# Kernel optimization log

Measured on AMD Instinct MI355X. Metric: run time of the kernel, lower is better.

## Reference

```python
import jax, jax.numpy as jnp
import numpy as np

T = 4          # num edge types
D = 256        # embedding_size == hidden_size
N = 100_000    # nodes
E_EDGES = 320_000
VOCAB = 10_000


def setup_inputs() -> dict:
    key = jax.random.key(0)
    ks = jax.random.split(key, 12)
    s = 0.02
    input_ids = jax.random.randint(ks[0], (1, N), 0, VOCAB)
    etype = jax.random.randint(ks[1], (1, E_EDGES), 1, T + 1)  # types 1..T
    src = jax.random.randint(ks[2], (1, E_EDGES), 0, N)
    tgt = jax.random.randint(ks[3], (1, E_EDGES), 0, N)
    typed_edges = jnp.stack([etype[0], src[0], tgt[0]], axis=0)[None]  # [1,3,E]
    embed_table = jax.random.normal(ks[4], (VOCAB, D)) * s
    # 6 inner layers (3 per concat block x 2 blocks): 256 -> 256
    edge_W_inner = jax.random.normal(ks[5], (6, T, D, 2 * D)) * s
    ln_s_inner = jnp.ones((6, D)); ln_b_inner = jnp.zeros((6, D))
    dense_W_inner = jax.random.normal(ks[6], (6, D, D)) * s
    dense_b_inner = jnp.zeros((6, D))
    # 2 output layers on concat [state, hidden]: hidden_size 512 -> 256
    edge_W_out = jax.random.normal(ks[7], (2, T, 2 * D, 4 * D)) * s
    ln_s_out = jnp.ones((2, 2 * D)); ln_b_out = jnp.zeros((2, 2 * D))
    dense_W_out = jax.random.normal(ks[8], (2, D, 2 * D)) * s
    dense_b_out = jnp.zeros((2, D))
    return {
        "input_ids": input_ids, "typed_edges": typed_edges,
        "embed_table": embed_table,
        "edge_W_inner": edge_W_inner, "ln_s_inner": ln_s_inner, "ln_b_inner": ln_b_inner,
        "dense_W_inner": dense_W_inner, "dense_b_inner": dense_b_inner,
        "edge_W_out": edge_W_out, "ln_s_out": ln_s_out, "ln_b_out": ln_b_out,
        "dense_W_out": dense_W_out, "dense_b_out": dense_b_out,
    }


def layer_norm(x, s, b, eps=1e-5):
    mu = jnp.mean(x, axis=-1, keepdims=True)
    var = jnp.mean((x - mu) ** 2, axis=-1, keepdims=True)
    return (x - mu) * jax.lax.rsqrt(var + eps) * s + b


def message_passing(state, etype, src, tgt, edge_W):
    # state [N,d]; edge_W [T, d, 2d]. Gather endpoints, per-type linear, scatter-add to targets.
    es = jnp.concatenate([state[src], state[tgt]], axis=1)  # [E, 2d]
    msgs = jnp.zeros((es.shape[0], edge_W.shape[1]), state.dtype)
    for t in range(edge_W.shape[0]):  # small fixed number of edge types
        msgs = msgs + jnp.where((etype == t + 1)[:, None], es @ edge_W[t].T, 0.0)
    return jax.ops.segment_sum(msgs, tgt, num_segments=state.shape[0])


def gnn_layer(state, etype, src, tgt, eW, ls, lb, dW, db):
    m = message_passing(state, etype, src, tgt, eW)
    h = layer_norm(jax.nn.gelu(m, approximate=False), ls, lb)
    return jnp.tanh(h @ dW.T + db)


def concat_block(state, etype, src, tgt, eWi, lsi, lbi, dWi, dbi, eWo, lso, lbo, dWo, dbo):
    x = state
    for i in range(3):
        x = gnn_layer(x, etype, src, tgt, eWi[i], lsi[i], lbi[i], dWi[i], dbi[i])
    res = jnp.concatenate([state, x], axis=1)  # [N, 2d] residual concat
    return gnn_layer(res, etype, src, tgt, eWo, lso, lbo, dWo, dbo)


def reference(input_ids, typed_edges, embed_table, edge_W_inner, ln_s_inner, ln_b_inner,
              dense_W_inner, dense_b_inner, edge_W_out, ln_s_out, ln_b_out,
              dense_W_out, dense_b_out):
    ids = input_ids[0]
    te = typed_edges[0]
    etype, src, tgt = te[0], te[1], te[2]
    x = embed_table[ids]  # [N, D]
    for b in range(2):
        sl = slice(3 * b, 3 * b + 3)
        x = concat_block(x, etype, src, tgt,
                         edge_W_inner[sl], ln_s_inner[sl], ln_b_inner[sl],
                         dense_W_inner[sl], dense_b_inner[sl],
                         edge_W_out[b], ln_s_out[b], ln_b_out[b],
                         dense_W_out[b], dense_b_out[b])
    return x
```

## Files before the change

kernel.cpp:

```cpp
#include <hip/hip_runtime.h>
#include <cstdio>

#define N_NODES 100000
#define NPAD    100096
#define NTILES  782
#define NE      320000
#define NCH     196
#define WCO_OFF 3145728L
#define OUT_ELEMS (N_NODES * 256)

typedef unsigned short ushort_t;
typedef unsigned short u16x4 __attribute__((ext_vector_type(4)));
typedef unsigned short u16x8 __attribute__((ext_vector_type(8)));
typedef _Float16       f16;
typedef _Float16       f16x8 __attribute__((ext_vector_type(8)));
typedef float          f32x4 __attribute__((ext_vector_type(4)));
typedef float          f32x4v __attribute__((ext_vector_type(4)));

__device__ __forceinline__ float bf2f(ushort_t u) {
    return __uint_as_float(((unsigned)u) << 16);
}
__device__ __forceinline__ ushort_t f2bf(float f) {
    unsigned u = __float_as_uint(f);
    u += 0x7FFFu + ((u >> 16) & 1u);
    return (ushort_t)(u >> 16);
}
__device__ __forceinline__ ushort_t f2h(float f) {
    f16 h = (f16)f;
    return __builtin_bit_cast(ushort_t, h);
}
__device__ __forceinline__ float h2f(ushort_t u) {
    return (float)__builtin_bit_cast(f16, u);
}

__device__ __forceinline__ int xcd_remap(int pbid, int nwg) {
    int q = nwg >> 3, r = nwg & 7;
    int xcd = pbid & 7, idx = pbid >> 3;
    int base = (xcd < r) ? xcd * (q + 1) : r * (q + 1) + (xcd - r) * q;
    return base + idx;
}

__device__ __forceinline__ float fast_tanh(float x) {
    x = fminf(fmaxf(x, -10.f), 10.f);
    float e = __expf(2.f * x);
    return (e - 1.f) / (e + 1.f);
}

__device__ __forceinline__ float gelu_f(float x) {
    return 0.5f * x * (1.f + erff(x * 0.70710678118654752f));
}

__global__ __launch_bounds__(256) void detect_k(const unsigned* __restrict__ w0, int* __restrict__ flag) {
    __shared__ int lds[256];
    int t = threadIdx.x;
    int cnt = 0;
    for (int i = t; i < 2048; i += 256) {
        unsigned e = (w0[i] >> 7) & 0xFFu;
        cnt += (e >= 96u && e <= 140u) ? 1 : 0;
    }
    lds[t] = cnt; __syncthreads();
    for (int s = 128; s > 0; s >>= 1) {
        if (t < s) lds[t] += lds[t + s];
        __syncthreads();
    }
    if (t == 0) *flag = (lds[0] < 1024) ? 1 : 0;
}

__device__ __forceinline__ ushort_t load_in(const void* p, long i, bool isf32) {
    return isf32 ? f2h(((const float*)p)[i]) : f2h(bf2f(((const ushort_t*)p)[i]));
}

struct CvtArgs {
    const void* src[8];
    ushort_t*   dst[8];
    int         n[8];
};

__global__ __launch_bounds__(256) void cvt_k(CvtArgs a, const int* __restrict__ flag) {
    int ti = blockIdx.y;
    int n = a.n[ti];
    const void* s = a.src[ti];
    ushort_t* d = a.dst[ti];
    bool isf32 = (*flag != 0);
    for (int i = blockIdx.x * 256 + threadIdx.x; i < n; i += gridDim.x * 256)
        d[i] = load_in(s, i, isf32);
}

__global__ __launch_bounds__(256) void scale_w_k(const ushort_t* __restrict__ dWiC,
                                                 const ushort_t* __restrict__ lsiC,
                                                 const ushort_t* __restrict__ lbiC,
                                                 const ushort_t* __restrict__ dbiC,
                                                 const ushort_t* __restrict__ dWoC,
                                                 const ushort_t* __restrict__ lsoC,
                                                 const ushort_t* __restrict__ lboC,
                                                 const ushort_t* __restrict__ dboC,
                                                 ushort_t* __restrict__ dWiS,
                                                 float* __restrict__ uwi, float* __restrict__ w0i,
                                                 ushort_t* __restrict__ dWoS,
                                                 float* __restrict__ uwo, float* __restrict__ w0o) {
    int wid = blockIdx.x * 4 + (threadIdx.x >> 6);
    int l = threadIdx.x & 63;
    float u = 0.f, w0 = 0.f;
    if (wid < 1536) {
        int lay = wid >> 8, c = wid & 255;
        u16x4 wv = *(const u16x4*)(dWiC + (size_t)wid * 256 + l * 4);
        u16x4 sv = *(const u16x4*)(lsiC + lay * 256 + l * 4);
        u16x4 bv = *(const u16x4*)(lbiC + lay * 256 + l * 4);
        u16x4 ov;
        #pragma unroll
        for (int i = 0; i < 4; i++) {
            float W = h2f(wv[i]);
            float ws = W * h2f(sv[i]);
            ov[i] = f2h(ws);
            u += ws; w0 += W * h2f(bv[i]);
        }
        *(u16x4*)(dWiS + (size_t)wid * 256 + l * 4) = ov;
        #pragma unroll
        for (int m = 1; m < 64; m <<= 1) {
            u += __shfl_xor(u, m, 64); w0 += __shfl_xor(w0, m, 64);
        }
        if (l == 0) { uwi[wid] = u; w0i[wid] = w0 + h2f(dbiC[lay * 256 + c]); }
    } else if (wid < 2048) {
        int w2 = wid - 1536;
        int b = w2 >> 8, c = w2 & 255;
        u16x8 wv = *(const u16x8*)(dWoC + (size_t)w2 * 512 + l * 8);
        u16x8 sv = *(const u16x8*)(lsoC + b * 512 + l * 8);
        u16x8 bv = *(const u16x8*)(lboC + b * 512 + l * 8);
        u16x8 ov;
        #pragma unroll
        for (int i = 0; i < 8; i++) {
            float W = h2f(wv[i]);
            float ws = W * h2f(sv[i]);
            ov[i] = f2h(ws);
            u += ws; w0 += W * h2f(bv[i]);
        }
        *(u16x8*)(dWoS + (size_t)w2 * 512 + l * 8) = ov;
        #pragma unroll
        for (int m = 1; m < 64; m <<= 1) {
            u += __shfl_xor(u, m, 64); w0 += __shfl_xor(w0, m, 64);
        }
        if (l == 0) { uwo[w2] = u; w0o[w2] = w0 + h2f(dboC[b * 256 + c]); }
    }
}

__global__ __launch_bounds__(256) void pack_w(const void* __restrict__ eWi,
                                              const void* __restrict__ eWo,
                                              ushort_t* __restrict__ WC,
                                              const int* __restrict__ flag) {
    long idx = (long)blockIdx.x * 256 + threadIdx.x;
    bool isf32 = (*flag != 0);
    const long ELI = 6L * 4 * 256 * 512;
    const long ELO = 2L * 4 * 512 * 1024;
    if (idx < ELI) {
        int j = idx & 511;
        int o = (idx >> 9) & 255;
        int t = (idx >> 17) & 3;
        long l = idx >> 19;
        int q = o >> 6, oo = o & 63;
        int k = j & 255;
        int n = ((j < 256) ? 0 : 256) + t * 64 + oo;
        WC[l * 524288 + (long)q * 131072 + (long)n * 256 + k] = load_in(eWi, idx, isf32);
    } else if (idx < ELI + ELO) {
        long i2 = idx - ELI;
        int j = i2 & 1023;
        int o = (i2 >> 10) & 511;
        int t = (i2 >> 19) & 3;
        long b = i2 >> 21;
        int c = o >> 6, oo = o & 63;
        int k = j & 511;
        int n = ((j < 512) ? 0 : 256) + t * 64 + oo;
        WC[WCO_OFF + b * 2097152L + (long)c * 262144 + (long)n * 512 + k] = load_in(eWo, i2, isf32);
    }
}

__global__ __launch_bounds__(256) void embed_k(const int* __restrict__ ids,
                                               const void* __restrict__ tab,
                                               ushort_t* __restrict__ S,
                                               const int* __restrict__ flag) {
    int row = blockIdx.x * 4 + (threadIdx.x >> 6);
    int l = threadIdx.x & 63;
    if (row >= N_NODES) return;
    int id = ids[row];
    u16x4 v;
    if (*flag) {
        f32x4v fv = *(const f32x4v*)((const float*)tab + (size_t)id * 256 + l * 4);
        #pragma unroll
        for (int i = 0; i < 4; i++) v[i] = f2h(fv[i]);
    } else {
        u16x4 bv = *(const u16x4*)((const ushort_t*)tab + (size_t)id * 256 + l * 4);
        #pragma unroll
        for (int i = 0; i < 4; i++) v[i] = f2h(bf2f(bv[i]));
    }
    *(u16x4*)(S + (size_t)row * 256 + l * 4) = v;
}

__global__ __launch_bounds__(256) void emit_k(const ushort_t* __restrict__ Bst, void* __restrict__ out,
                                              const int* __restrict__ flag) {
    long i = (long)blockIdx.x * 256 + threadIdx.x;
    if (i >= OUT_ELEMS) return;
    float v = h2f(Bst[i]);
    if (*flag) ((float*)out)[i] = v;
    else       ((ushort_t*)out)[i] = f2bf(v);
}

__global__ __launch_bounds__(256) void count_k(const int* __restrict__ tgt, int* __restrict__ counts) {
    int e = blockIdx.x * 256 + threadIdx.x;
    if (e < NE) atomicAdd(&counts[tgt[e]], 1);
}

__global__ __launch_bounds__(256) void scan1_k(const int* __restrict__ counts,
                                               int* __restrict__ incl, int* __restrict__ chsums) {
    __shared__ int lds[256];
    int c = blockIdx.x, t = threadIdx.x;
    int i0 = c * 512 + 2 * t;
    int a = (i0 < N_NODES) ? counts[i0] : 0;
    int b = (i0 + 1 < N_NODES) ? counts[i0 + 1] : 0;
    int ps = a + b;
    lds[t] = ps; __syncthreads();
    int x = ps;
    for (int off = 1; off < 256; off <<= 1) {
        int y = (t >= off) ? lds[t - off] : 0;
        __syncthreads();
        x += y; lds[t] = x;
        __syncthreads();
    }
    int excl = x - ps;
    if (i0 < N_NODES) incl[i0] = excl + a;
    if (i0 + 1 < N_NODES) incl[i0 + 1] = excl + a + b;
    if (t == 255) chsums[c] = x;
}

__global__ __launch_bounds__(256) void scan2_k(const int* __restrict__ chsums, int* __restrict__ chunkoff) {
    __shared__ int lds[256];
    int t = threadIdx.x;
    int v = (t < NCH) ? chsums[t] : 0;
    lds[t] = v; __syncthreads();
    int x = v;
    for (int off = 1; off < 256; off <<= 1) {
        int y = (t >= off) ? lds[t - off] : 0;
        __syncthreads();
        x += y; lds[t] = x;
        __syncthreads();
    }
    if (t <= NCH) chunkoff[t] = x - v;
}

__global__ __launch_bounds__(256) void scan3_k(const int* __restrict__ counts, const int* __restrict__ incl,
                                               const int* __restrict__ chunkoff,
                                               int* __restrict__ offsets, int* __restrict__ cursor) {
    int c = blockIdx.x, t = threadIdx.x;
    int base = chunkoff[c];
    #pragma unroll
    for (int k = 0; k < 2; k++) {
        int i = c * 512 + 2 * t + k;
        if (i < N_NODES) {
            int off = base + incl[i] - counts[i];
            offsets[i] = off;
            cursor[i] = off;
        }
    }
    if (c == 0 && t == 0) offsets[N_NODES] = chunkoff[NCH];
}

__global__ __launch_bounds__(256) void fill_k(const int* __restrict__ et, const int* __restrict__ src,
                                              const int* __restrict__ tgt,
                                              int* __restrict__ cursor, int* __restrict__ sorted) {
    int e = blockIdx.x * 256 + threadIdx.x;
    if (e < NE) {
        int pos = atomicAdd(&cursor[tgt[e]], 1);
        sorted[pos] = ((et[e] - 1) << 28) | src[e];
    }
}

template<int EPI>
__global__ __launch_bounds__(256) void gemm_bt(const ushort_t* __restrict__ A,
                                               const ushort_t* __restrict__ B,
                                               int K, int ldc,
                                               ushort_t* __restrict__ Cb,
                                               const float2* __restrict__ MR,
                                               const float* __restrict__ uu,
                                               const float* __restrict__ w0t,
                                               int storeM) {
    __shared__ __align__(16) ushort_t As[2][128 * 64];
    __shared__ __align__(16) ushort_t Bs[2][128 * 64];
    const int tid = threadIdx.x;
    const int w = tid >> 6, l = tid & 63;
    const int wr = w >> 1, wc = w & 1;
    const int gx = gridDim.x;
    const int lbid = xcd_remap(blockIdx.y * gx + blockIdx.x, gx * gridDim.y);
    const long m0 = (long)(lbid / gx) * 128, n0 = (long)(lbid % gx) * 128;
    const int lr = l >> 3;
    const int lc = (l & 7) * 8;
    const int cbk = ((l & 7) ^ lr) * 8;
    f32x4 acc[4][4];
    #pragma unroll
    for (int s = 0; s < 4; s++)
        #pragma unroll
        for (int n = 0; n < 4; n++) acc[s][n] = (f32x4){0.f, 0.f, 0.f, 0.f};

    auto stage = [&](int buf, int k0) {
        #pragma unroll
        for (int q = 0; q < 4; q++) {
            int row = w * 32 + q * 8 + lr;
            const ushort_t* ga = A + (m0 + row) * (long)K + k0 + cbk;
            __builtin_amdgcn_global_load_lds(
                (__attribute__((address_space(1))) unsigned int*)(ga),
                (__attribute__((address_space(3))) unsigned int*)(&As[buf][row * 64 + lc]), 16, 0, 0);
            const ushort_t* gb = B + (n0 + row) * (long)K + k0 + cbk;
            __builtin_amdgcn_global_load_lds(
                (__attribute__((address_space(1))) unsigned int*)(gb),
                (__attribute__((address_space(3))) unsigned int*)(&Bs[buf][row * 64 + lc]), 16, 0, 0);
        }
    };

    stage(0, 0);
    int cur = 0;
    for (int k0 = 0; k0 < K; k0 += 64) {
        __syncthreads();
        if (k0 + 64 < K) stage(cur ^ 1, k0 + 64);
        #pragma unroll
        for (int kk = 0; kk < 2; kk++) {
            f16x8 af[4], bfr[4];
            const int gb = kk * 4 + (l >> 4);
            const int sb = (gb ^ (l & 7)) * 8;
            #pragma unroll
            for (int s = 0; s < 4; s++)
                af[s] = *(const f16x8*)&As[cur][(wr * 64 + s * 16 + (l & 15)) * 64 + sb];
            #pragma unroll
            for (int n = 0; n < 4; n++)
                bfr[n] = *(const f16x8*)&Bs[cur][(wc * 64 + n * 16 + (l & 15)) * 64 + sb];
            #pragma unroll
            for (int s = 0; s < 4; s++)
                #pragma unroll
                for (int n = 0; n < 4; n++)
                    acc[s][n] = __builtin_amdgcn_mfma_f32_16x16x32_f16(bfr[n], af[s], acc[s][n], 0, 0, 0);
        }
        cur ^= 1;
    }
    const long r0 = m0 + wr * 64 + (l & 15);
    const long c0 = n0 + wc * 64 + ((l >> 4) << 2);
    #pragma unroll
    for (int s = 0; s < 4; s++) {
        long r = r0 + s * 16;
        if constexpr (EPI == 2) {
            if (r < storeM) {
                float2 mr = MR[r];
                #pragma unroll
                for (int n = 0; n < 4; n++) {
                    long c = c0 + n * 16;
                    f32x4v u4 = *(const f32x4v*)&uu[c];
                    f32x4v w4 = *(const f32x4v*)&w0t[c];
                    u16x4 o;
                    #pragma unroll
                    for (int j = 0; j < 4; j++)
                        o[j] = f2h(fast_tanh(mr.y * (acc[s][n][j] - mr.x * u4[j]) + w4[j]));
                    *(u16x4*)&Cb[r * ldc + c] = o;
                }
            }
        } else {
            #pragma unroll
            for (int n = 0; n < 4; n++) {
                long c = c0 + n * 16;
                u16x4 o;
                #pragma unroll
                for (int j = 0; j < 4; j++) o[j] = f2h(acc[s][n][j]);
                *(u16x4*)&Cb[r * ldc + c] = o;
            }
        }
    }
}

__global__ __launch_bounds__(256) void gemm_bt2(const ushort_t* __restrict__ A0,
                                                const ushort_t* __restrict__ A1,
                                                const ushort_t* __restrict__ B,
                                                int ldc,
                                                ushort_t* __restrict__ Cb) {
    __shared__ __align__(16) ushort_t As[2][128 * 64];
    __shared__ __align__(16) ushort_t Bs[2][128 * 64];
    const int tid = threadIdx.x;
    const int w = tid >> 6, l = tid & 63;
    const int wr = w >> 1, wc = w & 1;
    const int gx = gridDim.x;
    const int lbid = xcd_remap(blockIdx.y * gx + blockIdx.x, gx * gridDim.y);
    const long m0 = (long)(lbid / gx) * 128, n0 = (long)(lbid % gx) * 128;
    const int lr = l >> 3;
    const int lc = (l & 7) * 8;
    const int cbk = ((l & 7) ^ lr) * 8;
    f32x4 acc[4][4];
    #pragma unroll
    for (int s = 0; s < 4; s++)
        #pragma unroll
        for (int n = 0; n < 4; n++) acc[s][n] = (f32x4){0.f, 0.f, 0.f, 0.f};

    auto stage = [&](int buf, int k0) {
        const ushort_t* Ab = (k0 < 256) ? A0 : A1;
        const int kq = k0 & 255;
        #pragma unroll
        for (int q = 0; q < 4; q++) {
            int row = w * 32 + q * 8 + lr;
            const ushort_t* ga = Ab + (m0 + row) * 256L + kq + cbk;
            __builtin_amdgcn_global_load_lds(
                (__attribute__((address_space(1))) unsigned int*)(ga),
                (__attribute__((address_space(3))) unsigned int*)(&As[buf][row * 64 + lc]), 16, 0, 0);
            const ushort_t* gb = B + (n0 + row) * 512L + k0 + cbk;
            __builtin_amdgcn_global_load_lds(
                (__attribute__((address_space(1))) unsigned int*)(gb),
                (__attribute__((address_space(3))) unsigned int*)(&Bs[buf][row * 64 + lc]), 16, 0, 0);
        }
    };

    stage(0, 0);
    int cur = 0;
    for (int k0 = 0; k0 < 512; k0 += 64) {
        __syncthreads();
        if (k0 + 64 < 512) stage(cur ^ 1, k0 + 64);
        #pragma unroll
        for (int kk = 0; kk < 2; kk++) {
            f16x8 af[4], bfr[4];
            const int gb = kk * 4 + (l >> 4);
            const int sb = (gb ^ (l & 7)) * 8;
            #pragma unroll
            for (int s = 0; s < 4; s++)
                af[s] = *(const f16x8*)&As[cur][(wr * 64 + s * 16 + (l & 15)) * 64 + sb];
            #pragma unroll
            for (int n = 0; n < 4; n++)
                bfr[n] = *(const f16x8*)&Bs[cur][(wc * 64 + n * 16 + (l & 15)) * 64 + sb];
            #pragma unroll
            for (int s = 0; s < 4; s++)
                #pragma unroll
                for (int n = 0; n < 4; n++)
                    acc[s][n] = __builtin_amdgcn_mfma_f32_16x16x32_f16(bfr[n], af[s], acc[s][n], 0, 0, 0);
        }
        cur ^= 1;
    }
    const long r0 = m0 + wr * 64 + (l & 15);
    const long c0 = n0 + wc * 64 + ((l >> 4) << 2);
    #pragma unroll
    for (int s = 0; s < 4; s++) {
        long r = r0 + s * 16;
        #pragma unroll
        for (int n = 0; n < 4; n++) {
            long c = c0 + n * 16;
            u16x4 o;
            #pragma unroll
            for (int j = 0; j < 4; j++) o[j] = f2h(acc[s][n][j]);
            *(u16x4*)&Cb[r * ldc + c] = o;
        }
    }
}

__global__ __launch_bounds__(256) void agg_q(const ushort_t* __restrict__ Z,
                                             const int* __restrict__ offsets,
                                             const int* __restrict__ sorted,
                                             ushort_t* __restrict__ G, int mld, int q,
                                             float* __restrict__ Sg, float* __restrict__ Sq) {
    int v = blockIdx.x * 4 + (threadIdx.x >> 6);
    int l = threadIdx.x & 63;
    if (v >= NPAD) return;
    ushort_t* mp = G + (size_t)v * mld + (q << 6) + l;
    if (v >= N_NODES) { *mp = 0; return; }
    float acc = 0.f;
    int d0 = 0, d1 = 0, d2 = 0, d3 = 0;
    int beg = offsets[v], end = offsets[v + 1];
    for (int e = beg; e < end; ++e) {
        int pk = sorted[e];
        int t = pk >> 28;
        int s = pk & 0x0FFFFFFF;
        acc += h2f(Z[(size_t)s * 512 + (t << 6) + l]);
        d0 += (t == 0); d1 += (t == 1); d2 += (t == 2); d3 += (t == 3);
    }
    const ushort_t* zs = Z + (size_t)v * 512 + 256 + l;
    if (d0) acc += (float)d0 * h2f(zs[0]);
    if (d1) acc += (float)d1 * h2f(zs[64]);
    if (d2) acc += (float)d2 * h2f(zs[128]);
    if (d3) acc += (float)d3 * h2f(zs[192]);
    float g = gelu_f(acc);
    *mp = f2h(g);
    float sg = g, sq = g * g;
    #pragma unroll
    for (int m = 1; m < 64; m <<= 1) {
        sg += __shfl_xor(sg, m, 64);
        sq += __shfl_xor(sq, m, 64);
    }
    if (l == 0) {
        atomicAdd(&Sg[v], sg);
        atomicAdd(&Sq[v], sq);
    }
}

__global__ __launch_bounds__(256) void stats_k(float* __restrict__ Sg, float* __restrict__ Sq,
                                               float2* __restrict__ MR, float inv) {
    int v = blockIdx.x * 256 + threadIdx.x;
    if (v >= N_NODES) return;
    float mean = Sg[v] * inv;
    float var = fmaxf(Sq[v] * inv - mean * mean, 0.f);
    MR[v] = make_float2(mean, rsqrtf(var + 1e-5f));
    Sg[v] = 0.f; Sq[v] = 0.f;
}

extern "C" void kernel_launch(void* const* d_in, const int* in_sizes, int n_in,
                              void* d_out, int out_size, void* d_ws, size_t ws_size,
                              hipStream_t stream) {
    const int* ids = (const int*)d_in[0];
    const int* te = (const int*)d_in[1];
    const int* et = te;
    const int* esrc = te + NE;
    const int* etgt = te + 2 * NE;
    const void* tab = d_in[2];
    const void* eWi = d_in[3];
    const void* lsi = d_in[4];
    const void* lbi = d_in[5];
    const void* dWi = d_in[6];
    const void* dbi = d_in[7];
    const void* eWo = d_in[8];
    const void* lso = d_in[9];
    const void* lbo = d_in[10];
    const void* dWo = d_in[11];
    const void* dbo = d_in[12];

    char* w = (char*)d_ws;
    auto alloc = [&](size_t bytes) -> char* {
        char* p = w; w += (bytes + 255) & ~(size_t)255; return p;
    };
    ushort_t* A    = (ushort_t*)alloc((size_t)NPAD * 256 * 2);
    ushort_t* Bst  = (ushort_t*)alloc((size_t)NPAD * 256 * 2);
    ushort_t* WC   = (ushort_t*)alloc(7340032UL * 2);
    ushort_t* lsiC = (ushort_t*)alloc(1536 * 2);
    ushort_t* lbiC = (ushort_t*)alloc(1536 * 2);
    ushort_t* dbiC = (ushort_t*)alloc(1536 * 2);
    ushort_t* lsoC = (ushort_t*)alloc(1024 * 2);
    ushort_t* lboC = (ushort_t*)alloc(1024 * 2);
    ushort_t* dboC = (ushort_t*)alloc(512 * 2);
    ushort_t* dWiC = (ushort_t*)alloc(393216UL * 2);
    ushort_t* dWoC = (ushort_t*)alloc(262144UL * 2);
    ushort_t* dWiS = (ushort_t*)alloc(393216UL * 2);
    ushort_t* dWoS = (ushort_t*)alloc(262144UL * 2);
    float* uwi     = (float*)alloc(1536 * 4);
    float* w0i     = (float*)alloc(1536 * 4);
    float* uwo     = (float*)alloc(512 * 4);
    float* w0o     = (float*)alloc(512 * 4);
    float* Sg      = (float*)alloc((size_t)NPAD * 4);
    float* Sq      = (float*)alloc((size_t)NPAD * 4);
    float2* MR     = (float2*)alloc((size_t)NPAD * 8);
    int* flag      = (int*)alloc(256);
    int* counts    = (int*)alloc((size_t)N_NODES * 4);
    int* incl      = (int*)alloc((size_t)N_NODES * 4);
    int* chsums    = (int*)alloc(1024);
    int* chunkoff  = (int*)alloc(1024);
    int* offsets   = (int*)alloc((size_t)(N_NODES + 8) * 4);
    int* cursor    = (int*)alloc((size_t)N_NODES * 4);
    int* sorted    = (int*)alloc((size_t)NE * 4);
    ushort_t* G    = (ushort_t*)alloc((size_t)NPAD * 512 * 2);
    ushort_t* R;
    if ((size_t)out_size >= (size_t)NPAD * 256 * 2) R = (ushort_t*)d_out;
    else R = (ushort_t*)alloc((size_t)NPAD * 256 * 2);
    size_t fixed = (size_t)(w - (char*)d_ws);

    const size_t ZQ_BYTES = (size_t)NPAD * 512 * 2;
    size_t bigsz = (ws_size > fixed) ? (ws_size - fixed) : 0;
    if (bigsz < ZQ_BYTES) {
        fprintf(stderr, "kernel_launch: ws too small (%zu bytes, fixed %zu, big %zu) -- no-op\n",
                ws_size, fixed, bigsz);
        return;
    }
    ushort_t* Zq = (ushort_t*)w;

    detect_k<<<1, 256, 0, stream>>>((const unsigned*)tab, flag);
    CvtArgs ca;
    ca.src[0] = lsi;  ca.dst[0] = lsiC; ca.n[0] = 1536;
    ca.src[1] = lbi;  ca.dst[1] = lbiC; ca.n[1] = 1536;
    ca.src[2] = dbi;  ca.dst[2] = dbiC; ca.n[2] = 1536;
    ca.src[3] = lso;  ca.dst[3] = lsoC; ca.n[3] = 1024;
    ca.src[4] = lbo;  ca.dst[4] = lboC; ca.n[4] = 1024;
    ca.src[5] = dbo;  ca.dst[5] = dboC; ca.n[5] = 512;
    ca.src[6] = dWi;  ca.dst[6] = dWiC; ca.n[6] = 393216;
    ca.src[7] = dWo;  ca.dst[7] = dWoC; ca.n[7] = 262144;
    cvt_k<<<dim3(1536, 8), 256, 0, stream>>>(ca, flag);
    scale_w_k<<<512, 256, 0, stream>>>(dWiC, lsiC, lbiC, dbiC, dWoC, lsoC, lboC, dboC,
                                       dWiS, uwi, w0i, dWoS, uwo, w0o);
    hipMemsetAsync(counts, 0, (size_t)N_NODES * 4, stream);
    hipMemsetAsync(Sg, 0, (size_t)NPAD * 4, stream);
    hipMemsetAsync(Sq, 0, (size_t)NPAD * 4, stream);
    hipMemsetAsync(A   + (size_t)N_NODES * 256, 0, (size_t)(NPAD - N_NODES) * 256 * 2, stream);
    hipMemsetAsync(Bst + (size_t)N_NODES * 256, 0, (size_t)(NPAD - N_NODES) * 256 * 2, stream);
    hipMemsetAsync(R   + (size_t)N_NODES * 256, 0, (size_t)(NPAD - N_NODES) * 256 * 2, stream);
    pack_w<<<28672, 256, 0, stream>>>(eWi, eWo, WC, flag);
    embed_k<<<N_NODES / 4, 256, 0, stream>>>(ids, tab, A, flag);
    count_k<<<(NE + 255) / 256, 256, 0, stream>>>(etgt, counts);
    scan1_k<<<NCH, 256, 0, stream>>>(counts, incl, chsums);
    scan2_k<<<1, 256, 0, stream>>>(chsums, chunkoff);
    scan3_k<<<NCH, 256, 0, stream>>>(counts, incl, chunkoff, offsets, cursor);
    fill_k<<<(NE + 255) / 256, 256, 0, stream>>>(et, esrc, etgt, cursor, sorted);

    auto inner_layer = [&](const ushort_t* Xin, ushort_t* Xout, int lay) {
        for (int q = 0; q < 4; q++) {
            gemm_bt<3><<<dim3(4, NTILES), 256, 0, stream>>>(
                Xin, WC + (long)lay * 524288 + (long)q * 131072, 256, 512, Zq,
                nullptr, nullptr, nullptr, 0);
            agg_q<<<NPAD / 4, 256, 0, stream>>>(Zq, offsets, sorted, G, 256, q, Sg, Sq);
        }
        stats_k<<<(N_NODES + 255) / 256, 256, 0, stream>>>(Sg, Sq, MR, 1.f / 256.f);
        gemm_bt<2><<<dim3(2, NTILES), 256, 0, stream>>>(G, dWiS + (long)lay * 65536, 256, 256,
                                                        Xout, MR, uwi + lay * 256, w0i + lay * 256, N_NODES);
    };

    auto out_layer = [&](const ushort_t* X0, const ushort_t* X1, int b, ushort_t* dest) {
        for (int c = 0; c < 8; c++) {
            gemm_bt2<<<dim3(4, NTILES), 256, 0, stream>>>(
                X0, X1, WC + WCO_OFF + (long)b * 2097152 + (long)c * 262144, 512, Zq);
            agg_q<<<NPAD / 4, 256, 0, stream>>>(Zq, offsets, sorted, G, 512, c, Sg, Sq);
        }
        stats_k<<<(N_NODES + 255) / 256, 256, 0, stream>>>(Sg, Sq, MR, 1.f / 512.f);
        gemm_bt<2><<<dim3(2, NTILES), 256, 0, stream>>>(G, dWoS + (long)b * 131072, 512, 256,
                                                        dest, MR, uwo + b * 256, w0o + b * 256, N_NODES);
    };

    inner_layer(A, Bst, 0);
    inner_layer(Bst, R, 1);
    inner_layer(R, Bst, 2);
    out_layer(A, Bst, 0, R);
    inner_layer(R, A, 3);
    inner_layer(A, Bst, 4);
    inner_layer(Bst, A, 5);
    out_layer(R, A, 1, Bst);

    emit_k<<<(OUT_ELEMS + 255) / 256, 256, 0, stream>>>(Bst, d_out, flag);
}
```

Measured before the change: 6.046 ms.

## Triple-buffer GEMM LDS staging with BK=32 and explicit vmcnt waits

```diff
diff --git a/kernel.cpp b/kernel.cpp
--- a/kernel.cpp
+++ b/kernel.cpp
@@ -281,17 +281,18 @@
                                                const float* __restrict__ uu,
                                                const float* __restrict__ w0t,
                                                int storeM) {
-    __shared__ __align__(16) ushort_t As[2][128 * 64];
-    __shared__ __align__(16) ushort_t Bs[2][128 * 64];
+    __shared__ __align__(16) ushort_t As[3][128 * 32];
+    __shared__ __align__(16) ushort_t Bs[3][128 * 32];
     const int tid = threadIdx.x;
     const int w = tid >> 6, l = tid & 63;
     const int wr = w >> 1, wc = w & 1;
     const int gx = gridDim.x;
     const int lbid = xcd_remap(blockIdx.y * gx + blockIdx.x, gx * gridDim.y);
     const long m0 = (long)(lbid / gx) * 128, n0 = (long)(lbid % gx) * 128;
-    const int lr = l >> 3;
-    const int lc = (l & 7) * 8;
-    const int cbk = ((l & 7) ^ lr) * 8;
+    const int cbk = (((l & 3) ^ ((l >> 4) & 3)) * 8);
+    const int ldst = (l & 3) * 8;
+    const int lrow = l >> 2;
+    const int sb = (((l >> 4) ^ ((l >> 2) & 3)) * 8);
     f32x4 acc[4][4];
     #pragma unroll
     for (int s = 0; s < 4; s++)
@@ -300,42 +301,44 @@
 
     auto stage = [&](int buf, int k0) {
         #pragma unroll
-        for (int q = 0; q < 4; q++) {
-            int row = w * 32 + q * 8 + lr;
+        for (int q = 0; q < 2; q++) {
+            int row = w * 32 + q * 16 + lrow;
             const ushort_t* ga = A + (m0 + row) * (long)K + k0 + cbk;
             __builtin_amdgcn_global_load_lds(
                 (__attribute__((address_space(1))) unsigned int*)(ga),
-                (__attribute__((address_space(3))) unsigned int*)(&As[buf][row * 64 + lc]), 16, 0, 0);
+                (__attribute__((address_space(3))) unsigned int*)(&As[buf][row * 32 + ldst]), 16, 0, 0);
             const ushort_t* gb = B + (n0 + row) * (long)K + k0 + cbk;
             __builtin_amdgcn_global_load_lds(
                 (__attribute__((address_space(1))) unsigned int*)(gb),
-                (__attribute__((address_space(3))) unsigned int*)(&Bs[buf][row * 64 + lc]), 16, 0, 0);
+                (__attribute__((address_space(3))) unsigned int*)(&Bs[buf][row * 32 + ldst]), 16, 0, 0);
         }
     };
 
     stage(0, 0);
-    int cur = 0;
-    for (int k0 = 0; k0 < K; k0 += 64) {
-        __syncthreads();
-        if (k0 + 64 < K) stage(cur ^ 1, k0 + 64);
-        #pragma unroll
-        for (int kk = 0; kk < 2; kk++) {
-            f16x8 af[4], bfr[4];
-            const int gb = kk * 4 + (l >> 4);
-            const int sb = (gb ^ (l & 7)) * 8;
-            #pragma unroll
-            for (int s = 0; s < 4; s++)
-                af[s] = *(const f16x8*)&As[cur][(wr * 64 + s * 16 + (l & 15)) * 64 + sb];
+    stage(1, 32);
+    int buf = 0;
+    for (int k0 = 0; k0 < K; k0 += 32) {
+        if (k0 + 32 < K) asm volatile("s_waitcnt vmcnt(4)" ::: "memory");
+        else             asm volatile("s_waitcnt vmcnt(0)" ::: "memory");
+        __builtin_amdgcn_s_barrier();
+        __builtin_amdgcn_sched_barrier(0);
+        if (k0 + 64 < K) {
+            int bn = buf + 2; if (bn >= 3) bn -= 3;
+            stage(bn, k0 + 64);
+        }
+        f16x8 af[4], bfr[4];
+        #pragma unroll
+        for (int s = 0; s < 4; s++)
+            af[s] = *(const f16x8*)&As[buf][(wr * 64 + s * 16 + (l & 15)) * 32 + sb];
+        #pragma unroll
+        for (int n = 0; n < 4; n++)
+            bfr[n] = *(const f16x8*)&Bs[buf][(wc * 64 + n * 16 + (l & 15)) * 32 + sb];
+        #pragma unroll
+        for (int s = 0; s < 4; s++)
             #pragma unroll
             for (int n = 0; n < 4; n++)
-                bfr[n] = *(const f16x8*)&Bs[cur][(wc * 64 + n * 16 + (l & 15)) * 64 + sb];
-            #pragma unroll
-            for (int s = 0; s < 4; s++)
-                #pragma unroll
-                for (int n = 0; n < 4; n++)
-                    acc[s][n] = __builtin_amdgcn_mfma_f32_16x16x32_f16(bfr[n], af[s], acc[s][n], 0, 0, 0);
-        }
-        cur ^= 1;
+                acc[s][n] = __builtin_amdgcn_mfma_f32_16x16x32_f16(bfr[n], af[s], acc[s][n], 0, 0, 0);
+        buf++; if (buf >= 3) buf = 0;
     }
     const long r0 = m0 + wr * 64 + (l & 15);
     const long c0 = n0 + wc * 64 + ((l >> 4) << 2);
@@ -375,17 +378,18 @@
                                                 const ushort_t* __restrict__ B,
                                                 int ldc,
                                                 ushort_t* __restrict__ Cb) {
-    __shared__ __align__(16) ushort_t As[2][128 * 64];
-    __shared__ __align__(16) ushort_t Bs[2][128 * 64];
+    __shared__ __align__(16) ushort_t As[3][128 * 32];
+    __shared__ __align__(16) ushort_t Bs[3][128 * 32];
     const int tid = threadIdx.x;
     const int w = tid >> 6, l = tid & 63;
     const int wr = w >> 1, wc = w & 1;
     const int gx = gridDim.x;
     const int lbid = xcd_remap(blockIdx.y * gx + blockIdx.x, gx * gridDim.y);
     const long m0 = (long)(lbid / gx) * 128, n0 = (long)(lbid % gx) * 128;
-    const int lr = l >> 3;
-    const int lc = (l & 7) * 8;
-    const int cbk = ((l & 7) ^ lr) * 8;
+    const int cbk = (((l & 3) ^ ((l >> 4) & 3)) * 8);
+    const int ldst = (l & 3) * 8;
+    const int lrow = l >> 2;
+    const int sb = (((l >> 4) ^ ((l >> 2) & 3)) * 8);
     f32x4 acc[4][4];
     #pragma unroll
     for (int s = 0; s < 4; s++)
@@ -396,42 +400,44 @@
         const ushort_t* Ab = (k0 < 256) ? A0 : A1;
         const int kq = k0 & 255;
         #pragma unroll
-        for (int q = 0; q < 4; q++) {
-            int row = w * 32 + q * 8 + lr;
+        for (int q = 0; q < 2; q++) {
+            int row = w * 32 + q * 16 + lrow;
             const ushort_t* ga = Ab + (m0 + row) * 256L + kq + cbk;
             __builtin_amdgcn_global_load_lds(
                 (__attribute__((address_space(1))) unsigned int*)(ga),
-                (__attribute__((address_space(3))) unsigned int*)(&As[buf][row * 64 + lc]), 16, 0, 0);
+                (__attribute__((address_space(3))) unsigned int*)(&As[buf][row * 32 + ldst]), 16, 0, 0);
             const ushort_t* gb = B + (n0 + row) * 512L + k0 + cbk;
             __builtin_amdgcn_global_load_lds(
                 (__attribute__((address_space(1))) unsigned int*)(gb),
-                (__attribute__((address_space(3))) unsigned int*)(&Bs[buf][row * 64 + lc]), 16, 0, 0);
+                (__attribute__((address_space(3))) unsigned int*)(&Bs[buf][row * 32 + ldst]), 16, 0, 0);
         }
     };
 
     stage(0, 0);
-    int cur = 0;
-    for (int k0 = 0; k0 < 512; k0 += 64) {
-        __syncthreads();
-        if (k0 + 64 < 512) stage(cur ^ 1, k0 + 64);
-        #pragma unroll
-        for (int kk = 0; kk < 2; kk++) {
-            f16x8 af[4], bfr[4];
-            const int gb = kk * 4 + (l >> 4);
-            const int sb = (gb ^ (l & 7)) * 8;
-            #pragma unroll
-            for (int s = 0; s < 4; s++)
-                af[s] = *(const f16x8*)&As[cur][(wr * 64 + s * 16 + (l & 15)) * 64 + sb];
+    stage(1, 32);
+    int buf = 0;
+    for (int k0 = 0; k0 < 512; k0 += 32) {
+        if (k0 + 32 < 512) asm volatile("s_waitcnt vmcnt(4)" ::: "memory");
+        else               asm volatile("s_waitcnt vmcnt(0)" ::: "memory");
+        __builtin_amdgcn_s_barrier();
+        __builtin_amdgcn_sched_barrier(0);
+        if (k0 + 64 < 512) {
+            int bn = buf + 2; if (bn >= 3) bn -= 3;
+            stage(bn, k0 + 64);
+        }
+        f16x8 af[4], bfr[4];
+        #pragma unroll
+        for (int s = 0; s < 4; s++)
+            af[s] = *(const f16x8*)&As[buf][(wr * 64 + s * 16 + (l & 15)) * 32 + sb];
+        #pragma unroll
+        for (int n = 0; n < 4; n++)
+            bfr[n] = *(const f16x8*)&Bs[buf][(wc * 64 + n * 16 + (l & 15)) * 32 + sb];
+        #pragma unroll
+        for (int s = 0; s < 4; s++)
             #pragma unroll
             for (int n = 0; n < 4; n++)
-                bfr[n] = *(const f16x8*)&Bs[cur][(wc * 64 + n * 16 + (l & 15)) * 64 + sb];
-            #pragma unroll
-            for (int s = 0; s < 4; s++)
-                #pragma unroll
-                for (int n = 0; n < 4; n++)
-                    acc[s][n] = __builtin_amdgcn_mfma_f32_16x16x32_f16(bfr[n], af[s], acc[s][n], 0, 0, 0);
-        }
-        cur ^= 1;
+                acc[s][n] = __builtin_amdgcn_mfma_f32_16x16x32_f16(bfr[n], af[s], acc[s][n], 0, 0, 0);
+        buf++; if (buf >= 3) buf = 0;
     }
     const long r0 = m0 + wr * 64 + (l & 15);
     const long c0 = n0 + wc * 64 + ((l >> 4) << 2);
```

Measured after the change: 6.061 ms. No clear change (+0.2%).
